# Kernel tuning notes

Hardware: AMD Instinct MI355X
Metric: run time of the kernel (lower is better)

The kernel has to match this reference:

```python
import jax, jax.numpy as jnp
import numpy as np

DELTA = 1e-6
B, INPUT, N, WL, R = 32, 1024, 1024, 64, 4
IFACE = WL * R + 3 * WL + 5 * R + 3  # 471


def setup_inputs() -> dict:
    key = jax.random.key(0)
    ks = jax.random.split(key, 9)
    return {
        "x": jax.random.normal(ks[0], (B, INPUT), jnp.float32),
        "W_if": jax.random.normal(ks[1], (INPUT, IFACE), jnp.float32) * 0.02,
        "b_if": jnp.zeros((IFACE,), jnp.float32),
        "memory": jax.random.normal(ks[2], (B, N, WL), jnp.float32) * 0.1,
        "link_matrix": jax.random.uniform(ks[3], (B, 1, N, N), jnp.float32) * 1e-3,
        "precedence": jax.random.uniform(ks[4], (B, 1, N), jnp.float32) * 1e-2,
        "read_weights": jax.random.uniform(ks[5], (B, R, N), jnp.float32) / N,
        "write_weights": jax.random.uniform(ks[6], (B, 1, N), jnp.float32) / N,
        "usage": jax.random.uniform(ks[7], (B, N), jnp.float32),
    }


def _content(memory, keys, strengths):
    # cosine-similarity content addressing; memory [b,N,W], keys [b,h,W]
    mn = memory / (jnp.linalg.norm(memory, axis=-1, keepdims=True) + DELTA)
    kn = keys / (jnp.linalg.norm(keys, axis=-1, keepdims=True) + DELTA)
    sim = jnp.einsum('bhw,bnw->bhn', kn, mn)
    return jax.nn.softmax(sim * strengths[..., None], axis=-1)


def reference(x, W_if, b_if, memory, link_matrix, precedence, read_weights, write_weights, usage):
    b = x.shape[0]
    xi = x @ W_if + b_if  # [b, IFACE]

    # --- parse interface vector (offsets per the torch module) ---
    o = 0
    read_keys = jnp.tanh(xi[:, o:o + R * WL].reshape(b, R, WL)); o += R * WL
    read_strengths = jax.nn.softplus(xi[:, o:o + R]); o += R            # [b,r]
    write_key = jnp.tanh(xi[:, o:o + WL].reshape(b, 1, WL)); o += WL
    write_strength = jax.nn.softplus(xi[:, o:o + 1]); o += 1            # [b,1]
    erase_vector = jax.nn.sigmoid(xi[:, o:o + WL].reshape(b, 1, WL)); o += WL
    write_vector = jnp.tanh(xi[:, o:o + WL].reshape(b, 1, WL)); o += WL
    free_gates = jax.nn.sigmoid(xi[:, o:o + R]); o += R                 # [b,r]
    allocation_gate = jax.nn.sigmoid(xi[:, o:o + 1]); o += 1            # [b,1]
    write_gate = jax.nn.sigmoid(xi[:, o:o + 1]); o += 1                 # [b,1]
    read_modes = jax.nn.softmax(xi[:, o:o + 3 * R].reshape(b, R, 3), axis=-1)

    # --- write phase ---
    wcw = _content(memory, write_key, write_strength)  # [b,1,N]

    # usage update
    u = usage + (1.0 - usage) * (1.0 - jnp.prod(1.0 - write_weights, axis=1))
    psi = jnp.prod(1.0 - free_gates[:, :, None] * read_weights, axis=1)
    u = u * psi

    # allocation via ascending sort + exclusive cumprod, then unsort
    u = DELTA + (1.0 - DELTA) * u
    perm = jnp.argsort(u, axis=1)                       # ascending usage order (phi)
    sorted_u = jnp.take_along_axis(u, perm, axis=1)
    ones_col = jnp.ones((b, 1), u.dtype)
    prod_su = jnp.cumprod(jnp.concatenate([ones_col, sorted_u], axis=1), axis=1)[:, :-1]
    sorted_alloc = (1.0 - sorted_u) * prod_su
    inv_perm = jnp.argsort(perm, axis=1)                # phi_rev: inverse permutation
    alloc = jnp.take_along_axis(sorted_alloc, inv_perm, axis=1)[:, None, :]  # [b,1,N]

    # write weighting
    ag = allocation_gate[..., None]
    wg = write_gate[..., None]
    ww = wg * (ag * alloc + (1.0 - ag) * wcw)           # [b,1,N]

    # memory erase + write (h = 1 write head)
    new_memory = memory * (1.0 - jnp.einsum('bhn,bhw->bnw', ww, erase_vector)) \
                 + jnp.einsum('bhn,bhw->bnw', ww, write_vector)

    # link matrix update (NxN outer-product, zero diagonal)
    ww_i = ww[:, :, :, None]                            # [b,1,N,1]
    ww_j = ww[:, :, None, :]                            # [b,1,1,N]
    prec_j = precedence[:, :, None, :]                  # [b,1,1,N]
    new_link = (1.0 - ww_i - ww_j) * link_matrix + ww_i * prec_j
    eye_mask = 1.0 - jnp.eye(N, dtype=new_link.dtype)
    new_link = new_link * eye_mask[None, None, :, :]

    # precedence update
    new_prec = (1.0 - jnp.sum(ww, axis=-1, keepdims=True)) * precedence + ww

    # --- read phase ---
    fwd_w = jnp.einsum('bhij,brj->bri', new_link, read_weights)   # forward links
    bwd_w = jnp.einsum('bhji,brj->bri', new_link, read_weights)   # backward links
    crw = _content(new_memory, read_keys, read_strengths)         # [b,r,N]
    new_rw = read_modes[..., 0:1] * bwd_w + read_modes[..., 1:2] * crw + read_modes[..., 2:3] * fwd_w
    read_vectors = jnp.einsum('brn,bnw->brw', new_rw, new_memory)  # [b,r,W]
    return read_vectors
```

## Files before the change

kernel.cpp:

```cpp
#include <hip/hip_runtime.h>
#include <math.h>

#define DELTA_ 1e-6f
#define IFACE_ 471
#define XI_STRIDE 480

#define OFF_XI    0
#define OFF_RKN   15360
#define OFF_RS    23552
#define OFF_ER    23680
#define OFF_WV    25728
#define OFF_RM    27776
#define OFF_WW    28160
#define OFF_WWRW  60928
#define OFF_PRD   192000
#define OFF_WRD   192128
#define OFF_INVN  192256
#define OFF_DIAG  225024
#define OFF_NM    257792
#define OFF_RAP   2354944
#define OFF_RBP   2617088
#define OFF_SAP   2879232
#define OFF_SBP   4976384

__device__ __forceinline__ float sigm_(float x){ return 1.f/(1.f+expf(-x)); }
__device__ __forceinline__ float softp_(float x){ return fmaxf(x,0.f)+log1pf(expf(-fabsf(x))); }
__device__ __forceinline__ float dot4_(float4 a, float4 b){ return a.x*b.x+a.y*b.y+a.z*b.z+a.w*b.w; }

__global__ __launch_bounds__(256) void k_xi(const float* __restrict__ x,
    const float* __restrict__ W, const float* __restrict__ bias,
    float* __restrict__ xi) {
  int b = blockIdx.x;
  int j0 = blockIdx.y*64;
  int t = threadIdx.x;
  int jl = t & 63, kq = t >> 6;
  __shared__ __align__(16) float sx[1024];
  __shared__ float s_part[256];
  for (int q=t; q<256; q+=256) ((float4*)sx)[q] = ((const float4*)(x + b*1024))[q];
  __syncthreads();
  int j = j0 + jl;
  int jc = j < IFACE_ ? j : IFACE_-1;
  float acc = 0.f;
  const float* Wp = W + (size_t)kq*256*IFACE_ + jc;
  #pragma unroll 4
  for (int k=0;k<256;++k) acc += sx[kq*256+k]*Wp[(size_t)k*IFACE_];
  s_part[t] = acc;
  __syncthreads();
  if (t < 64 && (j0+t) < IFACE_) {
    xi[b*XI_STRIDE + j0+t] = s_part[t]+s_part[64+t]+s_part[128+t]+s_part[192+t] + bias[j0+t];
  }
}

__global__ __launch_bounds__(256) void k_batch(
    const float* __restrict__ xi, const float* __restrict__ memory,
    const float* __restrict__ usage, const float* __restrict__ read_w,
    const float* __restrict__ write_w, const float* __restrict__ precedence,
    float* __restrict__ rkn, float* __restrict__ rs, float* __restrict__ er,
    float* __restrict__ wv, float* __restrict__ rm, float* __restrict__ ww_out,
    float* __restrict__ wwrw, float* __restrict__ prd, float* __restrict__ wrd) {
  int b = blockIdx.x; int t = threadIdx.x;
  int lane = t & 63; int wave = t >> 6;
  __shared__ float s_act[472];
  __shared__ __align__(16) float s_key[64];
  __shared__ float s_wcw[1024];
  __shared__ unsigned long long s_k64[1024];
  __shared__ float s_ps[1024];
  __shared__ float s_alloc[1024];
  __shared__ float s_red[32];
  __shared__ float s_bc[2];

  for (int q = t; q < IFACE_; q += 256) {
    float v = xi[b*XI_STRIDE+q];
    float a;
    if      (q < 256) a = tanhf(v);
    else if (q < 260) a = softp_(v);
    else if (q < 324) a = tanhf(v);
    else if (q < 325) a = softp_(v);
    else if (q < 389) a = sigm_(v);
    else if (q < 453) a = tanhf(v);
    else if (q < 459) a = sigm_(v);
    else              a = v;
    s_act[q] = a;
  }
  __syncthreads();
  if (t < 4) {
    float m0=s_act[459+3*t], m1=s_act[460+3*t], m2=s_act[461+3*t];
    float mx=fmaxf(m0,fmaxf(m1,m2));
    float e0=expf(m0-mx), e1=expf(m1-mx), e2=expf(m2-mx);
    float s=e0+e1+e2;
    rm[b*12+3*t+0]=e0/s; rm[b*12+3*t+1]=e1/s; rm[b*12+3*t+2]=e2/s;
  }
  if (t < 64) { er[b*64+t]=s_act[325+t]; wv[b*64+t]=s_act[389+t]; }
  {
    int r = wave;
    float v = s_act[r*64+lane];
    float ss = v*v;
    for (int off=32; off; off>>=1) ss += __shfl_xor(ss, off);
    rkn[((size_t)b*4+r)*64+lane] = v / (sqrtf(ss)+DELTA_);
    if (lane==0) rs[b*4+r] = s_act[256+r];
  }
  if (wave==0) {
    float v = s_act[260+lane];
    float ss=v*v;
    for (int off=32; off; off>>=1) ss += __shfl_xor(ss, off);
    s_key[lane] = v/(sqrtf(ss)+DELTA_);
  }
  __syncthreads();
  float wstr = s_act[324], agv = s_act[457], wgv = s_act[458];

  for (int n=t; n<1024; n+=256) {
    const float4* row = (const float4*)(memory + ((size_t)b*1024+n)*64);
    float dot=0.f, nn2=0.f;
    #pragma unroll
    for (int w4=0; w4<16; ++w4) {
      float4 m4 = row[w4];
      float4 k4 = ((const float4*)s_key)[w4];
      dot += dot4_(m4,k4);
      nn2 += dot4_(m4,m4);
    }
    s_wcw[n] = dot/(sqrtf(nn2)+DELTA_) * wstr;
  }
  __syncthreads();
  {
    float lm=-1e30f;
    for (int n=t;n<1024;n+=256) lm=fmaxf(lm,s_wcw[n]);
    for (int off=32;off;off>>=1) lm=fmaxf(lm,__shfl_xor(lm,off));
    if (lane==0) s_red[wave]=lm;
    __syncthreads();
    if (t==0) s_bc[0]=fmaxf(fmaxf(s_red[0],s_red[1]),fmaxf(s_red[2],s_red[3]));
    __syncthreads();
    float mx=s_bc[0], ls=0.f;
    for (int n=t;n<1024;n+=256){ float e=expf(s_wcw[n]-mx); s_wcw[n]=e; ls+=e; }
    for (int off=32;off;off>>=1) ls+=__shfl_xor(ls,off);
    if (lane==0) s_red[wave]=ls;
    __syncthreads();
    if (t==0) s_bc[1]=s_red[0]+s_red[1]+s_red[2]+s_red[3];
    __syncthreads();
    float inv=1.f/s_bc[1];
    for (int n=t;n<1024;n+=256) s_wcw[n]*=inv;
  }
  __syncthreads();

  for (int n=t; n<1024; n+=256) {
    float us = usage[b*1024+n];
    float wwi = write_w[b*1024+n];
    float u = us + (1.f-us)*wwi;
    float psi = 1.f;
    #pragma unroll
    for (int r=0;r<4;++r) psi *= (1.f - s_act[453+r]*read_w[((size_t)b*4+r)*1024+n]);
    u *= psi;
    u = DELTA_ + (1.f-DELTA_)*u;
    unsigned int ub = __float_as_uint(u);
    s_k64[n] = ((unsigned long long)ub<<32) | (unsigned int)n;
  }

  for (int k=2; k<=1024; k<<=1) {
    for (int j=k>>1; j>0; j>>=1) {
      __syncthreads();
      for (int idx=t; idx<1024; idx+=256) {
        int partner = idx ^ j;
        if (partner > idx) {
          unsigned long long a=s_k64[idx], c=s_k64[partner];
          bool asc = ((idx & k) == 0);
          bool sw = asc ? (a > c) : (a < c);
          if (sw) { s_k64[idx]=c; s_k64[partner]=a; }
        }
      }
    }
  }
  __syncthreads();

  for (int n=t;n<1024;n+=256) s_ps[n] = __uint_as_float((unsigned int)(s_k64[n]>>32));
  __syncthreads();
  for (int off=1; off<1024; off<<=1) {
    float tmp[4];
    #pragma unroll
    for (int m=0;m<4;++m){ int n=t+256*m; tmp[m] = (n>=off)? s_ps[n-off] : 1.f; }
    __syncthreads();
    #pragma unroll
    for (int m=0;m<4;++m){ int n=t+256*m; s_ps[n] *= tmp[m]; }
    __syncthreads();
  }
  for (int n=t;n<1024;n+=256) {
    unsigned long long kv = s_k64[n];
    float su = __uint_as_float((unsigned int)(kv>>32));
    int oi = (int)(kv & 0xffffffffu);
    float prod = (n==0)?1.f:s_ps[n-1];
    s_alloc[oi] = (1.f-su)*prod;
  }
  __syncthreads();

  float pp[4]={0,0,0,0}, wp[4]={0,0,0,0};
  for (int n=t;n<1024;n+=256) {
    float w_ = wgv*(agv*s_alloc[n] + (1.f-agv)*s_wcw[n]);
    ww_out[b*1024+n]=w_;
    float pn = precedence[b*1024+n];
    #pragma unroll
    for (int r=0;r<4;++r){
      float rwv = read_w[((size_t)b*4+r)*1024+n];
      wwrw[((size_t)b*4+r)*1024+n] = w_*rwv;
      pp[r] += pn*rwv;
      wp[r] += w_*rwv;
    }
  }
  #pragma unroll
  for (int r=0;r<4;++r){
    for (int off=32;off;off>>=1){ pp[r]+=__shfl_xor(pp[r],off); wp[r]+=__shfl_xor(wp[r],off); }
  }
  if (lane==0){
    #pragma unroll
    for (int r=0;r<4;++r){ s_red[wave*8+r]=pp[r]; s_red[wave*8+4+r]=wp[r]; }
  }
  __syncthreads();
  if (t<4)              prd[b*4+t]   = s_red[t]+s_red[8+t]+s_red[16+t]+s_red[24+t];
  else if (t<8){ int r=t-4; wrd[b*4+r] = s_red[4+r]+s_red[12+r]+s_red[20+r]+s_red[28+r]; }
}

__global__ __launch_bounds__(256) void k_newmem(const float* __restrict__ memory,
    const float* __restrict__ ww, const float* __restrict__ er,
    const float* __restrict__ wv, float* __restrict__ newmem, float* __restrict__ invn) {
  int b = blockIdx.x;
  int n0 = blockIdx.y*64;
  int t = threadIdx.x;
  int lane16 = t & 15, rl = t >> 4;
  __shared__ float s_ww[64];
  __shared__ __align__(16) float s_er[64];
  __shared__ __align__(16) float s_wv[64];
  if (t < 64) s_ww[t] = ww[b*1024 + n0 + t];
  else if (t < 128) s_er[t-64] = er[b*64 + (t-64)];
  else if (t < 192) s_wv[t-128] = wv[b*64 + (t-128)];
  __syncthreads();
  float4 e4 = ((const float4*)s_er)[lane16];
  float4 v4 = ((const float4*)s_wv)[lane16];
  #pragma unroll
  for (int p=0;p<4;++p) {
    int rloc = p*16 + rl;
    int row = n0 + rloc;
    float wn = s_ww[rloc];
    size_t i4 = ((size_t)b*1024+row)*16 + lane16;
    float4 m4 = ((const float4*)memory)[i4];
    float4 nv;
    nv.x = m4.x*(1.f-wn*e4.x) + wn*v4.x;
    nv.y = m4.y*(1.f-wn*e4.y) + wn*v4.y;
    nv.z = m4.z*(1.f-wn*e4.z) + wn*v4.z;
    nv.w = m4.w*(1.f-wn*e4.w) + wn*v4.w;
    ((float4*)newmem)[i4] = nv;
    float ss = dot4_(nv,nv);
    ss += __shfl_xor(ss,1); ss += __shfl_xor(ss,2);
    ss += __shfl_xor(ss,4); ss += __shfl_xor(ss,8);
    if (lane16==0) invn[b*1024+row] = 1.f/(sqrtf(ss)+DELTA_);
  }
}

__global__ __launch_bounds__(256) void k_scan(const float* __restrict__ L,
    const float* __restrict__ read_w, const float* __restrict__ wwrw,
    float* __restrict__ RAp, float* __restrict__ RBp,
    float* __restrict__ SAp, float* __restrict__ SBp,
    float* __restrict__ diag) {
  int b = blockIdx.x, rc = blockIdx.y, cc = blockIdx.z;
  int i0 = rc*64;
  int q = threadIdx.x;
  int r = q>>6, lc = q&63;
  __shared__ __align__(16) float RM[64*68];
  __shared__ __align__(16) float CM[64*68];
  __shared__ __align__(16) float s_wc[256], s_uc[256];
  __shared__ __align__(16) float s_wr[256], s_ur[256];
  s_wr[q] = read_w[((size_t)b*4+r)*1024 + i0 + lc];
  s_ur[q] = wwrw  [((size_t)b*4+r)*1024 + i0 + lc];
  const float4* L4 = (const float4*)(L + (size_t)b*1048576);
  float4 pre[4]; float wpA, wpB;
  {
    int tc0 = cc*512;
    #pragma unroll
    for (int m=0;m<4;++m){
      int flat = q + 256*m;
      int row = flat>>4, c4 = flat&15;
      pre[m] = L4[(size_t)(i0+row)*256 + (tc0>>2) + c4];
    }
    wpA = read_w[((size_t)b*4+r)*1024 + tc0 + lc];
    wpB = wwrw  [((size_t)b*4+r)*1024 + tc0 + lc];
  }
  float pa=0.f, pb=0.f;
  for (int t=0;t<8;++t) {
    int tc0 = cc*512 + t*64;
    __syncthreads();
    #pragma unroll
    for (int m=0;m<4;++m){
      int flat = q + 256*m;
      int row = flat>>4, c4 = flat&15;
      ((float4*)RM)[row*17 + c4] = pre[m];
      const float* p = (const float*)&pre[m];
      #pragma unroll
      for (int j=0;j<4;++j) CM[(4*c4+j)*68 + row] = p[j];
    }
    s_wc[q] = wpA; s_uc[q] = wpB;
    __syncthreads();
    if (t<7){
      int nc0 = tc0 + 64;
      #pragma unroll
      for (int m=0;m<4;++m){
        int flat = q + 256*m;
        int row = flat>>4, c4 = flat&15;
        pre[m] = L4[(size_t)(i0+row)*256 + (nc0>>2) + c4];
      }
      wpA = read_w[((size_t)b*4+r)*1024 + nc0 + lc];
      wpB = wwrw  [((size_t)b*4+r)*1024 + nc0 + lc];
    }
    if (i0 == tc0 && q < 64) diag[b*1024 + i0 + q] = RM[q*68 + q];
    {
      const float4* RM4 = (const float4*)RM;
      const float4* w4p = (const float4*)(s_wc + r*64);
      const float4* u4p = (const float4*)(s_uc + r*64);
      #pragma unroll
      for (int c4=0;c4<16;++c4){
        float4 a4 = RM4[lc*17 + c4];
        pa += dot4_(a4, w4p[c4]);
        pb += dot4_(a4, u4p[c4]);
      }
    }
    {
      const float4* CM4 = (const float4*)CM;
      const float4* w4p = (const float4*)(s_wr + r*64);
      const float4* u4p = (const float4*)(s_ur + r*64);
      float sa=0.f, sb=0.f;
      #pragma unroll
      for (int i4=0;i4<16;++i4){
        float4 c4v = CM4[lc*17 + i4];
        sa += dot4_(c4v, w4p[i4]);
        sb += dot4_(c4v, u4p[i4]);
      }
      SAp[(((size_t)(b*16+rc))*4+r)*1024 + tc0 + lc] = sa;
      SBp[(((size_t)(b*16+rc))*4+r)*1024 + tc0 + lc] = sb;
    }
  }
  RAp[(((size_t)(b*2+cc))*4+r)*1024 + i0 + lc] = pa;
  RBp[(((size_t)(b*2+cc))*4+r)*1024 + i0 + lc] = pb;
}

__global__ __launch_bounds__(256) void k_read(
    const float* __restrict__ newmem, const float* __restrict__ invn,
    const float* __restrict__ rkn, const float* __restrict__ rs,
    const float* __restrict__ rm, const float* __restrict__ RAp,
    const float* __restrict__ RBp, const float* __restrict__ SAp,
    const float* __restrict__ SBp, const float* __restrict__ ww,
    const float* __restrict__ precedence, const float* __restrict__ read_w,
    const float* __restrict__ diag, const float* __restrict__ prd,
    const float* __restrict__ wrd, float* __restrict__ out) {
  int b=blockIdx.x, r=blockIdx.y;
  int t=threadIdx.x, lane=t&63, wave=t>>6;
  int lane16 = t & 15, rl = t >> 4;
  __shared__ __align__(16) float s_key[64];
  __shared__ float s_arr[1024];
  __shared__ float s_red[4];
  __shared__ float s_bc[2];
  __shared__ __align__(16) float4 s_acc[16][16];
  if (t<64) s_key[t]=rkn[((size_t)b*4+r)*64+t];
  __syncthreads();
  float rstr = rs[b*4+r];
  float4 key4 = ((const float4*)s_key)[lane16];
  for (int p=0;p<64;++p) {
    int row = p*16 + rl;
    float4 m4 = ((const float4*)newmem)[((size_t)b*1024+row)*16 + lane16];
    float d = dot4_(m4, key4);
    d += __shfl_xor(d,1); d += __shfl_xor(d,2);
    d += __shfl_xor(d,4); d += __shfl_xor(d,8);
    if (lane16==0) s_arr[row] = d * invn[b*1024+row] * rstr;
  }
  __syncthreads();
  {
    float lm=-1e30f;
    for (int n=t;n<1024;n+=256) lm=fmaxf(lm,s_arr[n]);
    for (int off=32;off;off>>=1) lm=fmaxf(lm,__shfl_xor(lm,off));
    if (lane==0) s_red[wave]=lm;
    __syncthreads();
    if (t==0) s_bc[0]=fmaxf(fmaxf(s_red[0],s_red[1]),fmaxf(s_red[2],s_red[3]));
    __syncthreads();
    float mx=s_bc[0], ls=0.f;
    for (int n=t;n<1024;n+=256){ float e=expf(s_arr[n]-mx); s_arr[n]=e; ls+=e; }
    for (int off=32;off;off>>=1) ls+=__shfl_xor(ls,off);
    if (lane==0) s_red[wave]=ls;
    __syncthreads();
    if (t==0) s_bc[1]=s_red[0]+s_red[1]+s_red[2]+s_red[3];
    __syncthreads();
    float inv=1.f/s_bc[1];
    for (int n=t;n<1024;n+=256) s_arr[n]*=inv;
  }
  __syncthreads();
  float m0=rm[b*12+r*3+0], m1=rm[b*12+r*3+1], m2=rm[b*12+r*3+2];
  float pd=prd[b*4+r], wd=wrd[b*4+r];
  for (int n=t;n<1024;n+=256) {
    float ra=0.f, rb=0.f;
    #pragma unroll
    for (int cc=0;cc<2;++cc){
      ra += RAp[(((size_t)(b*2+cc))*4+r)*1024+n];
      rb += RBp[(((size_t)(b*2+cc))*4+r)*1024+n];
    }
    float sa=0.f, sb=0.f;
    #pragma unroll
    for (int rc=0;rc<16;++rc){
      sa+=SAp[(((size_t)(b*16+rc))*4+r)*1024+n];
      sb+=SBp[(((size_t)(b*16+rc))*4+r)*1024+n];
    }
    float w_ = ww[b*1024+n];
    float pn = precedence[b*1024+n];
    float rwv= read_w[((size_t)b*4+r)*1024+n];
    float dg = diag[b*1024+n];
    float fwd = (1.f-w_)*ra - rb + w_*pd - ((1.f-2.f*w_)*dg + w_*pn)*rwv;
    float bwd = (1.f-w_)*sa - sb + pn*(wd - w_*rwv) - (1.f-2.f*w_)*dg*rwv;
    float crw = s_arr[n];
    __syncthreads();
    s_arr[n] = m0*bwd + m1*crw + m2*fwd;
    __syncthreads();
  }
  __syncthreads();
  float4 acc = {0,0,0,0};
  for (int p=0;p<64;++p) {
    int row = p*16 + rl;
    float4 m4 = ((const float4*)newmem)[((size_t)b*1024+row)*16 + lane16];
    float s = s_arr[row];
    acc.x += s*m4.x; acc.y += s*m4.y; acc.z += s*m4.z; acc.w += s*m4.w;
  }
  s_acc[rl][lane16] = acc;
  __syncthreads();
  if (t < 16) {
    float4 tot = {0,0,0,0};
    #pragma unroll
    for (int g=0; g<16; ++g) {
      float4 v = s_acc[g][t];
      tot.x+=v.x; tot.y+=v.y; tot.z+=v.z; tot.w+=v.w;
    }
    ((float4*)(out + (b*4+r)*64))[t] = tot;
  }
}

extern "C" void kernel_launch(void* const* d_in, const int* in_sizes, int n_in,
                              void* d_out, int out_size, void* d_ws, size_t ws_size,
                              hipStream_t stream) {
  const float* x      = (const float*)d_in[0];
  const float* W_if   = (const float*)d_in[1];
  const float* b_if   = (const float*)d_in[2];
  const float* memory = (const float*)d_in[3];
  const float* link   = (const float*)d_in[4];
  const float* prec   = (const float*)d_in[5];
  const float* read_w = (const float*)d_in[6];
  const float* write_w= (const float*)d_in[7];
  const float* usage  = (const float*)d_in[8];
  float* out = (float*)d_out;
  float* ws = (float*)d_ws;

  float* xi   = ws + OFF_XI;
  float* rkn  = ws + OFF_RKN;
  float* rs   = ws + OFF_RS;
  float* er   = ws + OFF_ER;
  float* wv   = ws + OFF_WV;
  float* rm   = ws + OFF_RM;
  float* wwp  = ws + OFF_WW;
  float* wwrw = ws + OFF_WWRW;
  float* prd  = ws + OFF_PRD;
  float* wrd  = ws + OFF_WRD;
  float* invn = ws + OFF_INVN;
  float* diag = ws + OFF_DIAG;
  float* nm   = ws + OFF_NM;
  float* RAp  = ws + OFF_RAP;
  float* RBp  = ws + OFF_RBP;
  float* SAp  = ws + OFF_SAP;
  float* SBp  = ws + OFF_SBP;

  k_xi<<<dim3(32,8), 256, 0, stream>>>(x, W_if, b_if, xi);
  k_batch<<<dim3(32), 256, 0, stream>>>(xi, memory, usage, read_w, write_w, prec,
                                        rkn, rs, er, wv, rm, wwp, wwrw, prd, wrd);
  k_scan<<<dim3(32,16,2), 256, 0, stream>>>(link, read_w, wwrw, RAp, RBp, SAp, SBp, diag);
  k_newmem<<<dim3(32,16), 256, 0, stream>>>(memory, wwp, er, wv, nm, invn);
  k_read<<<dim3(32,4), 256, 0, stream>>>(nm, invn, rkn, rs, rm, RAp, RBp, SAp, SBp,
                                         wwp, prec, read_w, diag, prd, wrd, out);
}
```

Before: 372.3 us.

## Drop transposed LDS tile in link scan; reuse one tile for row and column products

```diff
diff --git a/kernel.cpp b/kernel.cpp
--- a/kernel.cpp
+++ b/kernel.cpp
@@ -260,81 +260,96 @@
   int b = blockIdx.x, rc = blockIdx.y, cc = blockIdx.z;
   int i0 = rc*64;
   int q = threadIdx.x;
-  int r = q>>6, lc = q&63;
+  int r = q>>6, lane = q&63;
+  int g = lane>>4, c4 = lane&15;
   __shared__ __align__(16) float RM[64*68];
-  __shared__ __align__(16) float CM[64*68];
-  __shared__ __align__(16) float s_wc[256], s_uc[256];
-  __shared__ __align__(16) float s_wr[256], s_ur[256];
-  s_wr[q] = read_w[((size_t)b*4+r)*1024 + i0 + lc];
-  s_ur[q] = wwrw  [((size_t)b*4+r)*1024 + i0 + lc];
+
   const float4* L4 = (const float4*)(L + (size_t)b*1048576);
-  float4 pre[4]; float wpA, wpB;
+  const float* wA = read_w + ((size_t)b*4+r)*1024;
+  const float* wB = wwrw   + ((size_t)b*4+r)*1024;
+
+  float wrA[16], wrB[16];
+  #pragma unroll
+  for (int it=0; it<16; ++it) {
+    wrA[it] = wA[i0 + 4*it + g];
+    wrB[it] = wB[i0 + 4*it + g];
+  }
+
+  float ra[16], rb[16];
+  #pragma unroll
+  for (int it=0; it<16; ++it) { ra[it]=0.f; rb[it]=0.f; }
+
+  float4 pre[4];
   {
     int tc0 = cc*512;
     #pragma unroll
     for (int m=0;m<4;++m){
       int flat = q + 256*m;
-      int row = flat>>4, c4 = flat&15;
-      pre[m] = L4[(size_t)(i0+row)*256 + (tc0>>2) + c4];
-    }
-    wpA = read_w[((size_t)b*4+r)*1024 + tc0 + lc];
-    wpB = wwrw  [((size_t)b*4+r)*1024 + tc0 + lc];
-  }
-  float pa=0.f, pb=0.f;
+      int row = flat>>4, cq = flat&15;
+      pre[m] = L4[(size_t)(i0+row)*256 + (tc0>>2) + cq];
+    }
+  }
   for (int t=0;t<8;++t) {
     int tc0 = cc*512 + t*64;
+    float4 wcA = *(const float4*)(wA + tc0 + 4*c4);
+    float4 wcB = *(const float4*)(wB + tc0 + 4*c4);
     __syncthreads();
     #pragma unroll
     for (int m=0;m<4;++m){
       int flat = q + 256*m;
-      int row = flat>>4, c4 = flat&15;
-      ((float4*)RM)[row*17 + c4] = pre[m];
-      const float* p = (const float*)&pre[m];
-      #pragma unroll
-      for (int j=0;j<4;++j) CM[(4*c4+j)*68 + row] = p[j];
-    }
-    s_wc[q] = wpA; s_uc[q] = wpB;
+      int row = flat>>4, cq = flat&15;
+      ((float4*)RM)[row*17 + cq] = pre[m];
+    }
     __syncthreads();
     if (t<7){
       int nc0 = tc0 + 64;
       #pragma unroll
       for (int m=0;m<4;++m){
         int flat = q + 256*m;
-        int row = flat>>4, c4 = flat&15;
-        pre[m] = L4[(size_t)(i0+row)*256 + (nc0>>2) + c4];
+        int row = flat>>4, cq = flat&15;
+        pre[m] = L4[(size_t)(i0+row)*256 + (nc0>>2) + cq];
       }
-      wpA = read_w[((size_t)b*4+r)*1024 + nc0 + lc];
-      wpB = wwrw  [((size_t)b*4+r)*1024 + nc0 + lc];
     }
     if (i0 == tc0 && q < 64) diag[b*1024 + i0 + q] = RM[q*68 + q];
-    {
-      const float4* RM4 = (const float4*)RM;
-      const float4* w4p = (const float4*)(s_wc + r*64);
-      const float4* u4p = (const float4*)(s_uc + r*64);
-      #pragma unroll
-      for (int c4=0;c4<16;++c4){
-        float4 a4 = RM4[lc*17 + c4];
-        pa += dot4_(a4, w4p[c4]);
-        pb += dot4_(a4, u4p[c4]);
-      }
-    }
-    {
-      const float4* CM4 = (const float4*)CM;
-      const float4* w4p = (const float4*)(s_wr + r*64);
-      const float4* u4p = (const float4*)(s_ur + r*64);
-      float sa=0.f, sb=0.f;
-      #pragma unroll
-      for (int i4=0;i4<16;++i4){
-        float4 c4v = CM4[lc*17 + i4];
-        sa += dot4_(c4v, w4p[i4]);
-        sb += dot4_(c4v, u4p[i4]);
-      }
-      SAp[(((size_t)(b*16+rc))*4+r)*1024 + tc0 + lc] = sa;
-      SBp[(((size_t)(b*16+rc))*4+r)*1024 + tc0 + lc] = sb;
-    }
-  }
-  RAp[(((size_t)(b*2+cc))*4+r)*1024 + i0 + lc] = pa;
-  RBp[(((size_t)(b*2+cc))*4+r)*1024 + i0 + lc] = pb;
+    float4 sa = {0.f,0.f,0.f,0.f}, sb = {0.f,0.f,0.f,0.f};
+    #pragma unroll
+    for (int it=0; it<16; ++it) {
+      float4 cell = ((const float4*)RM)[(4*it+g)*17 + c4];
+      ra[it] += dot4_(cell, wcA);
+      rb[it] += dot4_(cell, wcB);
+      float a_ = wrA[it], b_ = wrB[it];
+      sa.x += cell.x*a_; sa.y += cell.y*a_; sa.z += cell.z*a_; sa.w += cell.w*a_;
+      sb.x += cell.x*b_; sb.y += cell.y*b_; sb.z += cell.z*b_; sb.w += cell.w*b_;
+    }
+    #pragma unroll
+    for (int off=32; off>=16; off>>=1) {
+      sa.x += __shfl_xor(sa.x,off); sa.y += __shfl_xor(sa.y,off);
+      sa.z += __shfl_xor(sa.z,off); sa.w += __shfl_xor(sa.w,off);
+      sb.x += __shfl_xor(sb.x,off); sb.y += __shfl_xor(sb.y,off);
+      sb.z += __shfl_xor(sb.z,off); sb.w += __shfl_xor(sb.w,off);
+    }
+    if (g==0) {
+      size_t base = (((size_t)(b*16+rc))*4+r)*1024 + tc0;
+      ((float4*)(SAp + base))[c4] = sa;
+      ((float4*)(SBp + base))[c4] = sb;
+    }
+  }
+  #pragma unroll
+  for (int it=0; it<16; ++it) {
+    #pragma unroll
+    for (int off=1; off<=8; off<<=1) {
+      ra[it] += __shfl_xor(ra[it],off);
+      rb[it] += __shfl_xor(rb[it],off);
+    }
+  }
+  if (c4==0) {
+    size_t baseA = (((size_t)(b*2+cc))*4+r)*1024 + i0;
+    #pragma unroll
+    for (int it=0; it<16; ++it) {
+      RAp[baseA + 4*it + g] = ra[it];
+      RBp[baseA + 4*it + g] = rb[it];
+    }
+  }
 }
 
 __global__ __launch_bounds__(256) void k_read(
@@ -408,9 +423,7 @@
     float fwd = (1.f-w_)*ra - rb + w_*pd - ((1.f-2.f*w_)*dg + w_*pn)*rwv;
     float bwd = (1.f-w_)*sa - sb + pn*(wd - w_*rwv) - (1.f-2.f*w_)*dg*rwv;
     float crw = s_arr[n];
-    __syncthreads();
     s_arr[n] = m0*bwd + m1*crw + m2*fwd;
-    __syncthreads();
   }
   __syncthreads();
   float4 acc = {0,0,0,0};
```

New measurement: 417.7 us. 1.12x slower.
